# Kernel tuning notes

Measured on AMD Instinct MI355X. Metric: run time of the kernel, lower is better.

Reference implementation:

```python
import jax, jax.numpy as jnp
import numpy as np

IN_CHS = 512
RED_CHS = int(IN_CHS * 0.25)  # 128
NUM_ACTIONS = 2
BATCH = 131072


def setup_inputs() -> dict:
    key = jax.random.key(0)
    kx, k1, k2 = jax.random.split(key, 3)
    x = jax.random.normal(kx, (BATCH, IN_CHS), dtype=jnp.float32)
    # conv_reduce: Linear(in_chs, reduced_chs), conv_expand: Linear(reduced_chs, 2)
    W1 = jax.random.normal(k1, (IN_CHS, RED_CHS), dtype=jnp.float32) * 0.02
    b1 = jnp.zeros((RED_CHS,), dtype=jnp.float32)
    W2 = jax.random.normal(k2, (RED_CHS, NUM_ACTIONS), dtype=jnp.float32) * 0.02
    b2 = jnp.zeros((NUM_ACTIONS,), dtype=jnp.float32)
    return {"x": x, "W1": W1, "b1": b1, "W2": W2, "b2": b2}


def reference(x, W1, b1, W2, b2):
    # tiny 2-layer MLP head
    h = jax.nn.relu(x @ W1 + b1)                 # [B, 128]
    logits = h @ W2 + b2                         # [B, 2]
    logp = jax.nn.log_softmax(logits, axis=1)    # softmax(dim=1) in log space
    # per-row categorical sampling (np.random.choice(p=attn[id])) via Gumbel-max,
    # fused instead of a Python loop with host sync
    skey = jax.random.fold_in(jax.random.key(0), 12345)
    g = jax.random.gumbel(skey, logp.shape, dtype=logp.dtype)
    actions = jnp.argmax(logp + g, axis=1).astype(jnp.int32)  # [B]
    return actions
```

## Files before the change

kernel.cpp:

```cpp
#include <hip/hip_runtime.h>
#include <stdint.h>
#include <math.h>


#define BM 128
#define BK 32
#define LDK 40
#define IN_CHS 512
#define RED_CHS 128
#define BATCH 131072

typedef __attribute__((ext_vector_type(8))) short bf16x8;
typedef __attribute__((ext_vector_type(4))) float f32x4;

__host__ __device__ inline void tf2x32(uint32_t k0, uint32_t k1,
                                       uint32_t x0, uint32_t x1,
                                       uint32_t* o0, uint32_t* o1) {
  uint32_t ks2 = k0 ^ k1 ^ 0x1BD11BDAu;
  x0 += k0; x1 += k1;
#define TFR(r) { x0 += x1; x1 = (x1 << r) | (x1 >> (32 - r)); x1 ^= x0; }
  TFR(13) TFR(15) TFR(26) TFR(6)
  x0 += k1; x1 += ks2 + 1u;
  TFR(17) TFR(29) TFR(16) TFR(24)
  x0 += ks2; x1 += k0 + 2u;
  TFR(13) TFR(15) TFR(26) TFR(6)
  x0 += k0; x1 += k1 + 3u;
  TFR(17) TFR(29) TFR(16) TFR(24)
  x0 += k1; x1 += ks2 + 4u;
  TFR(13) TFR(15) TFR(26) TFR(6)
  x0 += ks2; x1 += k0 + 5u;
#undef TFR
  *o0 = x0; *o1 = x1;
}

__device__ __forceinline__ float gumbel_from_bits(uint32_t bits) {
  uint32_t fb = (bits >> 9) | 0x3f800000u;
  float u = __uint_as_float(fb) - 1.0f;
  if (u == 0.0f) u = 1.175494350822287508e-38f;
  float t = -(float)log((double)u);
  return -(float)log((double)t);
}

__device__ __forceinline__ unsigned short f2bf(float f) {
  uint32_t u = __float_as_uint(f);
  return (unsigned short)((u + 0x7fffu + ((u >> 16) & 1u)) >> 16);
}
__device__ __forceinline__ float bf2f(unsigned short h) {
  return __uint_as_float(((uint32_t)h) << 16);
}

__global__ __launch_bounds__(256) void rl_head_mfma(
    const float* __restrict__ x, const float* __restrict__ W1,
    const float* __restrict__ b1, const float* __restrict__ W2,
    const float* __restrict__ b2, int* __restrict__ out,
    uint32_t fk0, uint32_t fk1) {
  __shared__ __align__(16) char smem[4 * BM * LDK * 2];
  unsigned short* Ah = (unsigned short*)smem;
  unsigned short* Al = Ah + BM * LDK;
  unsigned short* Bh = Al + BM * LDK;
  float* red = (float*)smem;

  const int tid = threadIdx.x;
  const int lane = tid & 63;
  const int w = tid >> 6;
  const int ln = lane & 15;
  const int quad = lane >> 4;
  const int row0 = blockIdx.x * BM;

  const int ar = tid >> 3;
  const int ak = (tid & 7) * 4;
  const int bc = tid & 127;
  const int bk0 = (tid >> 7) * 16;

  f32x4 acc[2][8];
#pragma unroll
  for (int i = 0; i < 2; ++i)
#pragma unroll
    for (int j = 0; j < 8; ++j) acc[i][j] = (f32x4)(0.0f);

  for (int kb = 0; kb < IN_CHS; kb += BK) {
    float4 av[4];
#pragma unroll
    for (int q = 0; q < 4; ++q)
      av[q] = *(const float4*)(&x[(size_t)(row0 + q * 32 + ar) * IN_CHS + kb + ak]);
    float bv[16];
#pragma unroll
    for (int i = 0; i < 16; ++i)
      bv[i] = W1[(size_t)(kb + bk0 + i) * RED_CHS + bc];

#pragma unroll
    for (int q = 0; q < 4; ++q) {
      const int r = q * 32 + ar;
      float f[4] = {av[q].x, av[q].y, av[q].z, av[q].w};
      ushort4 h4, l4;
      unsigned short* hp = (unsigned short*)&h4;
      unsigned short* lp = (unsigned short*)&l4;
#pragma unroll
      for (int c = 0; c < 4; ++c) {
        unsigned short h = f2bf(f[c]);
        hp[c] = h;
        lp[c] = f2bf(f[c] - bf2f(h));
      }
      *(ushort4*)(&Ah[r * LDK + ak]) = h4;
      *(ushort4*)(&Al[r * LDK + ak]) = l4;
    }
    {
      ushort4 h4[4], l4[4];
#pragma unroll
      for (int g = 0; g < 4; ++g) {
        unsigned short* hp = (unsigned short*)&h4[g];
        unsigned short* lp = (unsigned short*)&l4[g];
#pragma unroll
        for (int c = 0; c < 4; ++c) {
          float f = bv[g * 4 + c];
          unsigned short h = f2bf(f);
          hp[c] = h;
          lp[c] = f2bf(f - bf2f(h));
        }
      }
#pragma unroll
      for (int g = 0; g < 4; ++g) {
        *(ushort4*)(&Bh[bc * LDK + bk0 + g * 4]) = h4[g];
        *(ushort4*)(&Bh[BM * LDK + bc * LDK + bk0 + g * 4]) = l4[g];
      }
    }
    __syncthreads();

    const unsigned short* ap = &Ah[(w * 32 + ln) * LDK + quad * 8];
    bf16x8 ah0 = *(const bf16x8*)ap;
    bf16x8 ah1 = *(const bf16x8*)(ap + 16 * LDK);
    bf16x8 al0 = *(const bf16x8*)(ap + BM * LDK);
    bf16x8 al1 = *(const bf16x8*)(ap + BM * LDK + 16 * LDK);
#pragma unroll
    for (int ct = 0; ct < 8; ++ct) {
      const unsigned short* bp = &Bh[(ct * 16 + ln) * LDK + quad * 8];
      bf16x8 bh = *(const bf16x8*)bp;
      bf16x8 bl = *(const bf16x8*)(bp + BM * LDK);
      acc[0][ct] = __builtin_amdgcn_mfma_f32_16x16x32_bf16(ah0, bh, acc[0][ct], 0, 0, 0);
      acc[0][ct] = __builtin_amdgcn_mfma_f32_16x16x32_bf16(ah0, bl, acc[0][ct], 0, 0, 0);
      acc[0][ct] = __builtin_amdgcn_mfma_f32_16x16x32_bf16(al0, bh, acc[0][ct], 0, 0, 0);
      acc[0][ct] = __builtin_amdgcn_mfma_f32_16x16x32_bf16(al0, bl, acc[0][ct], 0, 0, 0);
      acc[1][ct] = __builtin_amdgcn_mfma_f32_16x16x32_bf16(ah1, bh, acc[1][ct], 0, 0, 0);
      acc[1][ct] = __builtin_amdgcn_mfma_f32_16x16x32_bf16(ah1, bl, acc[1][ct], 0, 0, 0);
      acc[1][ct] = __builtin_amdgcn_mfma_f32_16x16x32_bf16(al1, bh, acc[1][ct], 0, 0, 0);
      acc[1][ct] = __builtin_amdgcn_mfma_f32_16x16x32_bf16(al1, bl, acc[1][ct], 0, 0, 0);
    }
    __syncthreads();
  }

  float part[8][2];
#pragma unroll
  for (int s = 0; s < 8; ++s) { part[s][0] = 0.0f; part[s][1] = 0.0f; }
#pragma unroll
  for (int ct = 0; ct < 8; ++ct) {
    const int col = ct * 16 + ln;
    const float bb = b1[col];
    const float w20 = W2[col * 2 + 0];
    const float w21 = W2[col * 2 + 1];
#pragma unroll
    for (int rt = 0; rt < 2; ++rt)
#pragma unroll
      for (int reg = 0; reg < 4; ++reg) {
        float h = acc[rt][ct][reg] + bb;
        h = h > 0.0f ? h : 0.0f;
        part[rt * 4 + reg][0] = fmaf(h, w20, part[rt * 4 + reg][0]);
        part[rt * 4 + reg][1] = fmaf(h, w21, part[rt * 4 + reg][1]);
      }
  }
#pragma unroll
  for (int rt = 0; rt < 2; ++rt)
#pragma unroll
    for (int reg = 0; reg < 4; ++reg) {
      const int row = w * 32 + rt * 16 + quad * 4 + reg;
      red[(row * 2 + 0) * 17 + ln] = part[rt * 4 + reg][0];
      red[(row * 2 + 1) * 17 + ln] = part[rt * 4 + reg][1];
    }
  __syncthreads();

  if (tid < BM) {
    const int row = tid;
    float l0 = b2[0], l1 = b2[1];
#pragma unroll
    for (int c = 0; c < 16; ++c) {
      l0 += red[(row * 2 + 0) * 17 + c];
      l1 += red[(row * 2 + 1) * 17 + c];
    }
    float m = fmaxf(l0, l1);
    float s0 = l0 - m, s1 = l1 - m;
    float e0 = (float)exp((double)s0);
    float e1 = (float)exp((double)s1);
    float lse = (float)log((double)(e0 + e1));
    float lp0 = s0 - lse, lp1 = s1 - lse;
    const int gr = row0 + row;
    uint32_t a0, a1, c0, c1;
    tf2x32(fk0, fk1, 0u, (uint32_t)(2 * gr), &a0, &a1);
    tf2x32(fk0, fk1, 0u, (uint32_t)(2 * gr + 1), &c0, &c1);
    float g0 = gumbel_from_bits(a0 ^ a1);
    float g1 = gumbel_from_bits(c0 ^ c1);
    out[gr] = ((lp1 + g1) > (lp0 + g0)) ? 1 : 0;
  }
}

extern "C" void kernel_launch(void* const* d_in, const int* in_sizes, int n_in,
                              void* d_out, int out_size, void* d_ws,
                              size_t ws_size, hipStream_t stream) {
  (void)in_sizes; (void)n_in; (void)d_ws; (void)ws_size; (void)out_size;
  const float* x = (const float*)d_in[0];
  const float* W1 = (const float*)d_in[1];
  const float* b1 = (const float*)d_in[2];
  const float* W2 = (const float*)d_in[3];
  const float* b2 = (const float*)d_in[4];
  int* out = (int*)d_out;

  uint32_t fk0, fk1;
  tf2x32(0u, 0u, 0u, 12345u, &fk0, &fk1);

  dim3 grid(BATCH / BM);
  rl_head_mfma<<<grid, 256, 0, stream>>>(x, W1, b1, W2, b2, out, fk0, fk1);
}
```

Before: 370.3 us.

## Pre-split W1 into MFMA-ready bf16 hi/lo layout and double-buffer via direct LDS loads

A small prep kernel converts W1 once per call into bf16 hi/lo pairs laid out in MFMA fragment order in the workspace. The main kernel streams these tiles into double-buffered shared memory with global_load_lds, and loads x straight into registers in fragment layout, prefetching the next k-block. This removes the per-block W1 conversion and the shared-memory staging of A, and overlaps loads with MFMA work. The x hi part now uses truncation instead of rounding, which can change precision slightly. It also adds a second kernel launch and a launch-bounds occupancy hint.

```diff
diff --git a/kernel.cpp b/kernel.cpp
--- a/kernel.cpp
+++ b/kernel.cpp
@@ -4,11 +4,10 @@
 
 
 #define BM 128
-#define BK 32
-#define LDK 40
 #define IN_CHS 512
 #define RED_CHS 128
 #define BATCH 131072
+#define NKB 16
 
 typedef __attribute__((ext_vector_type(8))) short bf16x8;
 typedef __attribute__((ext_vector_type(4))) float f32x4;
@@ -49,16 +48,51 @@
   return __uint_as_float(((uint32_t)h) << 16);
 }
 
-__global__ __launch_bounds__(256) void rl_head_mfma(
-    const float* __restrict__ x, const float* __restrict__ W1,
+__global__ __launch_bounds__(256) void prep_w1(const float* __restrict__ W1,
+                                               unsigned short* __restrict__ wsB) {
+  const int idx = blockIdx.x * 256 + threadIdx.x;
+  const int lane = idx & 63;
+  const int ct = (idx >> 6) & 7;
+  const int kb = idx >> 9;
+  const int ln = lane & 15, quad = lane >> 4;
+  const int col = ct * 16 + ln;
+  const int k0 = kb * 32 + quad * 8;
+  ushort4 h[2], l[2];
+  unsigned short* hp = (unsigned short*)h;
+  unsigned short* lp = (unsigned short*)l;
+#pragma unroll
+  for (int j = 0; j < 8; ++j) {
+    float f = W1[(size_t)(k0 + j) * RED_CHS + col];
+    unsigned short hh = f2bf(f);
+    hp[j] = hh;
+    lp[j] = f2bf(f - bf2f(hh));
+  }
+  const size_t base = (size_t)kb * 8192 + (size_t)ct * 1024 + (size_t)lane * 8;
+  *(ushort4*)(&wsB[base + 0]) = h[0];
+  *(ushort4*)(&wsB[base + 4]) = h[1];
+  *(ushort4*)(&wsB[base + 512 + 0]) = l[0];
+  *(ushort4*)(&wsB[base + 512 + 4]) = l[1];
+}
+
+__device__ __forceinline__ void cvt_hilo8(const float4 p, const float4 q,
+                                          bf16x8* hi, bf16x8* lo) {
+  const float f[8] = {p.x, p.y, p.z, p.w, q.x, q.y, q.z, q.w};
+#pragma unroll
+  for (int c = 0; c < 8; ++c) {
+    const uint32_t u = __float_as_uint(f[c]);
+    (*hi)[c] = (short)(u >> 16);
+    const float r = f[c] - __uint_as_float(u & 0xffff0000u);
+    (*lo)[c] = (short)f2bf(r);
+  }
+}
+
+__global__ __launch_bounds__(256, 3) void rl_head_v2(
+    const float* __restrict__ x, const unsigned short* __restrict__ wsB,
     const float* __restrict__ b1, const float* __restrict__ W2,
     const float* __restrict__ b2, int* __restrict__ out,
     uint32_t fk0, uint32_t fk1) {
-  __shared__ __align__(16) char smem[4 * BM * LDK * 2];
-  unsigned short* Ah = (unsigned short*)smem;
-  unsigned short* Al = Ah + BM * LDK;
-  unsigned short* Bh = Al + BM * LDK;
-  float* red = (float*)smem;
+  __shared__ __align__(16) unsigned short Bs[2 * 8192];
+  float* red = (float*)Bs;
 
   const int tid = threadIdx.x;
   const int lane = tid & 63;
@@ -67,10 +101,8 @@
   const int quad = lane >> 4;
   const int row0 = blockIdx.x * BM;
 
-  const int ar = tid >> 3;
-  const int ak = (tid & 7) * 4;
-  const int bc = tid & 127;
-  const int bk0 = (tid >> 7) * 16;
+  const float* xp0 = &x[(size_t)(row0 + w * 32 + ln) * IN_CHS + quad * 8];
+  const float* xp1 = xp0 + (size_t)16 * IN_CHS;
 
   f32x4 acc[2][8];
 #pragma unroll
@@ -78,64 +110,47 @@
 #pragma unroll
     for (int j = 0; j < 8; ++j) acc[i][j] = (f32x4)(0.0f);
 
-  for (int kb = 0; kb < IN_CHS; kb += BK) {
-    float4 av[4];
-#pragma unroll
-    for (int q = 0; q < 4; ++q)
-      av[q] = *(const float4*)(&x[(size_t)(row0 + q * 32 + ar) * IN_CHS + kb + ak]);
-    float bv[16];
-#pragma unroll
-    for (int i = 0; i < 16; ++i)
-      bv[i] = W1[(size_t)(kb + bk0 + i) * RED_CHS + bc];
-
-#pragma unroll
-    for (int q = 0; q < 4; ++q) {
-      const int r = q * 32 + ar;
-      float f[4] = {av[q].x, av[q].y, av[q].z, av[q].w};
-      ushort4 h4, l4;
-      unsigned short* hp = (unsigned short*)&h4;
-      unsigned short* lp = (unsigned short*)&l4;
-#pragma unroll
-      for (int c = 0; c < 4; ++c) {
-        unsigned short h = f2bf(f[c]);
-        hp[c] = h;
-        lp[c] = f2bf(f[c] - bf2f(h));
-      }
-      *(ushort4*)(&Ah[r * LDK + ak]) = h4;
-      *(ushort4*)(&Al[r * LDK + ak]) = l4;
-    }
-    {
-      ushort4 h4[4], l4[4];
-#pragma unroll
-      for (int g = 0; g < 4; ++g) {
-        unsigned short* hp = (unsigned short*)&h4[g];
-        unsigned short* lp = (unsigned short*)&l4[g];
-#pragma unroll
-        for (int c = 0; c < 4; ++c) {
-          float f = bv[g * 4 + c];
-          unsigned short h = f2bf(f);
-          hp[c] = h;
-          lp[c] = f2bf(f - bf2f(h));
-        }
-      }
-#pragma unroll
-      for (int g = 0; g < 4; ++g) {
-        *(ushort4*)(&Bh[bc * LDK + bk0 + g * 4]) = h4[g];
-        *(ushort4*)(&Bh[BM * LDK + bc * LDK + bk0 + g * 4]) = l4[g];
-      }
-    }
+#define STAGE_B(kbn, nb)                                                         \
+  {                                                                              \
+    _Pragma("unroll") for (int r = 0; r < 4; ++r) {                              \
+      __builtin_amdgcn_global_load_lds(                                          \
+          (const __attribute__((address_space(1))) unsigned int*)(wsB +          \
+              ((size_t)(kbn)*8192 + (size_t)(r * 256 + tid) * 8)),               \
+          (__attribute__((address_space(3))) unsigned int*)(&Bs[(size_t)(nb)*    \
+              8192 + (size_t)(r * 256 + w * 64) * 8]),                           \
+          16, 0, 0);                                                             \
+    }                                                                            \
+  }
+
+  float4 ac0a, ac0b, ac1a, ac1b, an0a, an0b, an1a, an1b;
+
+  STAGE_B(0, 0);
+  ac0a = *(const float4*)(xp0 + 0);
+  ac0b = *(const float4*)(xp0 + 4);
+  ac1a = *(const float4*)(xp1 + 0);
+  ac1b = *(const float4*)(xp1 + 4);
+
+#pragma unroll 2
+  for (int kb = 0; kb < NKB; ++kb) {
+    const int cb = kb & 1;
+    if (kb + 1 < NKB) {
+      STAGE_B(kb + 1, cb ^ 1);
+      const float* p0 = xp0 + (kb + 1) * 32;
+      const float* p1 = xp1 + (kb + 1) * 32;
+      an0a = *(const float4*)(p0 + 0);
+      an0b = *(const float4*)(p0 + 4);
+      an1a = *(const float4*)(p1 + 0);
+      an1b = *(const float4*)(p1 + 4);
+    }
+    bf16x8 ah0, al0, ah1, al1;
+    cvt_hilo8(ac0a, ac0b, &ah0, &al0);
+    cvt_hilo8(ac1a, ac1b, &ah1, &al1);
     __syncthreads();
-
-    const unsigned short* ap = &Ah[(w * 32 + ln) * LDK + quad * 8];
-    bf16x8 ah0 = *(const bf16x8*)ap;
-    bf16x8 ah1 = *(const bf16x8*)(ap + 16 * LDK);
-    bf16x8 al0 = *(const bf16x8*)(ap + BM * LDK);
-    bf16x8 al1 = *(const bf16x8*)(ap + BM * LDK + 16 * LDK);
+    const unsigned short* Bb = &Bs[(size_t)cb * 8192];
 #pragma unroll
     for (int ct = 0; ct < 8; ++ct) {
-      const unsigned short* bp = &Bh[(ct * 16 + ln) * LDK + quad * 8];
-      bf16x8 bh = *(const bf16x8*)bp;
-      bf16x8 bl = *(const bf16x8*)(bp + BM * LDK);
+      bf16x8 bh = *(const bf16x8*)(Bb + ct * 1024 + lane * 8);
+      bf16x8 bl = *(const bf16x8*)(Bb + ct * 1024 + 512 + lane * 8);
       acc[0][ct] = __builtin_amdgcn_mfma_f32_16x16x32_bf16(ah0, bh, acc[0][ct], 0, 0, 0);
       acc[0][ct] = __builtin_amdgcn_mfma_f32_16x16x32_bf16(ah0, bl, acc[0][ct], 0, 0, 0);
       acc[0][ct] = __builtin_amdgcn_mfma_f32_16x16x32_bf16(al0, bh, acc[0][ct], 0, 0, 0);
@@ -146,7 +161,9 @@
       acc[1][ct] = __builtin_amdgcn_mfma_f32_16x16x32_bf16(al1, bl, acc[1][ct], 0, 0, 0);
     }
     __syncthreads();
-  }
+    ac0a = an0a; ac0b = an0b; ac1a = an1a; ac1b = an1b;
+  }
+#undef STAGE_B
 
   float part[8][2];
 #pragma unroll
@@ -204,17 +221,19 @@
 extern "C" void kernel_launch(void* const* d_in, const int* in_sizes, int n_in,
                               void* d_out, int out_size, void* d_ws,
                               size_t ws_size, hipStream_t stream) {
-  (void)in_sizes; (void)n_in; (void)d_ws; (void)ws_size; (void)out_size;
+  (void)in_sizes; (void)n_in; (void)ws_size; (void)out_size;
   const float* x = (const float*)d_in[0];
   const float* W1 = (const float*)d_in[1];
   const float* b1 = (const float*)d_in[2];
   const float* W2 = (const float*)d_in[3];
   const float* b2 = (const float*)d_in[4];
   int* out = (int*)d_out;
+  unsigned short* wsB = (unsigned short*)d_ws;
 
   uint32_t fk0, fk1;
   tf2x32(0u, 0u, 0u, 12345u, &fk0, &fk1);
 
-  dim3 grid(BATCH / BM);
-  rl_head_mfma<<<grid, 256, 0, stream>>>(x, W1, b1, W2, b2, out, fk0, fk1);
-}
+  prep_w1<<<dim3(32), 256, 0, stream>>>(W1, wsB);
+  rl_head_v2<<<dim3(BATCH / BM), 256, 0, stream>>>(x, wsB, b1, W2, b2,
+                                                   out, fk0, fk1);
+}
```

Result: no change. 374.4 us (+1.1%).
